# Kernel optimization log

Hardware: AMD Instinct MI355X
Metric: run time of the kernel (lower is better)

## Reference

```python
import jax, jax.numpy as jnp
import numpy as np

C = 256
C8 = C // 8
B, H, W = 8, 64, 64


def setup_inputs() -> dict:
    key = jax.random.key(0)
    ks = jax.random.split(key, 8)
    scale = 1.0 / np.sqrt(C)
    return {
        "x": jax.random.normal(ks[0], (B, C, H, W), dtype=jnp.float32),
        "wq": jax.random.normal(ks[1], (C8, C), dtype=jnp.float32) * scale,
        "bq": jax.random.normal(ks[2], (C8,), dtype=jnp.float32) * 0.01,
        "wk": jax.random.normal(ks[3], (C8, C), dtype=jnp.float32) * scale,
        "bk": jax.random.normal(ks[4], (C8,), dtype=jnp.float32) * 0.01,
        "wv": jax.random.normal(ks[5], (C, C), dtype=jnp.float32) * scale,
        "bv": jax.random.normal(ks[6], (C,), dtype=jnp.float32) * 0.01,
        "gamma": jax.random.normal(ks[7], (1,), dtype=jnp.float32) * 0.1,
    }


def reference(x, wq, bq, wk, bk, wv, bv, gamma):
    b, c, h, w = x.shape
    n = h * w
    xf = x.reshape(b, c, n)  # flatten spatial; 1x1 conv == channel matmul
    q = jnp.einsum('oc,bcn->bno', wq, xf) + bq            # [b, n, c/8]
    k = jnp.einsum('oc,bcn->bon', wk, xf) + bk[:, None]   # [b, c/8, n]
    v = jnp.einsum('oc,bcn->bon', wv, xf) + bv[:, None]   # [b, c, n]
    attn = jax.nn.softmax(jnp.einsum('bno,bom->bnm', q, k), axis=2)  # [b,n,n]
    out = jnp.einsum('bcm,bnm->bcn', v, attn).reshape(b, c, h, w)
    return x + gamma[0] * out
```

## Files before the change

### kernel.cpp

```cpp
#include <hip/hip_runtime.h>

typedef unsigned short ushort_t;
typedef __bf16 bf16x8 __attribute__((ext_vector_type(8)));
typedef float f32x16 __attribute__((ext_vector_type(16)));
typedef float f32x4 __attribute__((ext_vector_type(4)));
typedef unsigned int u32x4 __attribute__((ext_vector_type(4)));
typedef unsigned int u32x2 __attribute__((ext_vector_type(2)));

#define L2E 1.44269504088896340736f

__device__ __forceinline__ unsigned cvt_pk_bf16(float a, float b) {
  unsigned r;
  asm("v_cvt_pk_bf16_f32 %0, %1, %2" : "=v"(r) : "v"(a), "v"(b));
  return r;
}

__device__ __forceinline__ float fast_exp2(float v) {
#if __has_builtin(__builtin_amdgcn_exp2f)
  return __builtin_amdgcn_exp2f(v);
#else
  return exp2f(v);
#endif
}

__device__ __forceinline__ f32x16 mfma32(u32x4 a, u32x4 b, f32x16 c) {
  return __builtin_amdgcn_mfma_f32_32x32x16_bf16(
      __builtin_bit_cast(bf16x8, a), __builtin_bit_cast(bf16x8, b), c, 0, 0, 0);
}

__global__ __launch_bounds__(256, 1) void proj_kernel(
    const float* __restrict__ x,
    const float* __restrict__ wq, const float* __restrict__ bq,
    const float* __restrict__ wk, const float* __restrict__ bk,
    const float* __restrict__ wv, const float* __restrict__ bv,
    ushort_t* __restrict__ qtg, ushort_t* __restrict__ ktg,
    ushort_t* __restrict__ vtg)
{
  __shared__ ushort_t xT[128 * 256];
  __shared__ ushort_t wl[64 * 256];

  const int tid  = threadIdx.x;
  const int b    = blockIdx.x & 7;
  const int nt   = blockIdx.x >> 3;
  const int n0   = nt * 128;
  const int lane = tid & 63;
  const int wid  = tid >> 6;
  const int l31  = lane & 31;
  const int half = lane >> 5;

  {
    const int xn = tid & 127;
    const int ch = (tid >> 7) * 8;
    const float* xb = x + (size_t)b * 256 * 4096 + (n0 + xn);
    #pragma unroll
    for (int rep = 0; rep < 16; ++rep) {
      const int c0 = rep * 16 + ch;
      float f0 = xb[(size_t)(c0+0)*4096], f1 = xb[(size_t)(c0+1)*4096];
      float f2 = xb[(size_t)(c0+2)*4096], f3 = xb[(size_t)(c0+3)*4096];
      float f4 = xb[(size_t)(c0+4)*4096], f5 = xb[(size_t)(c0+5)*4096];
      float f6 = xb[(size_t)(c0+6)*4096], f7 = xb[(size_t)(c0+7)*4096];
      u32x4 pk;
      pk.x = cvt_pk_bf16(f0, f1); pk.y = cvt_pk_bf16(f2, f3);
      pk.z = cvt_pk_bf16(f4, f5); pk.w = cvt_pk_bf16(f6, f7);
      *(u32x4*)((char*)xT + xn*512 + ((c0*2) ^ ((xn & 7) << 4))) = pk;
    }
  }

  for (int oc = 0; oc < 5; ++oc) {
    __syncthreads();
    {
      const int r   = tid >> 2;
      const int row = oc*64 + r;
      const float* wrow = (row < 32) ? (wq + row*256)
                        : (row < 64) ? (wk + (row-32)*256)
                                     : (wv + (row-64)*256);
      #pragma unroll
      for (int rep = 0; rep < 4; ++rep) {
        const int c0 = ((tid & 3)*4 + rep) * 16;
        f32x4 g0 = *(const f32x4*)(wrow + c0);
        f32x4 g1 = *(const f32x4*)(wrow + c0 + 4);
        f32x4 g2 = *(const f32x4*)(wrow + c0 + 8);
        f32x4 g3 = *(const f32x4*)(wrow + c0 + 12);
        u32x4 pa, pb;
        pa.x = cvt_pk_bf16(g0.x, g0.y); pa.y = cvt_pk_bf16(g0.z, g0.w);
        pa.z = cvt_pk_bf16(g1.x, g1.y); pa.w = cvt_pk_bf16(g1.z, g1.w);
        pb.x = cvt_pk_bf16(g2.x, g2.y); pb.y = cvt_pk_bf16(g2.z, g2.w);
        pb.z = cvt_pk_bf16(g3.x, g3.y); pb.w = cvt_pk_bf16(g3.z, g3.w);
        *(u32x4*)((char*)wl + r*512 + ((c0*2)     ^ ((r & 7) << 4))) = pa;
        *(u32x4*)((char*)wl + r*512 + (((c0+8)*2) ^ ((r & 7) << 4))) = pb;
      }
    }
    __syncthreads();

    f32x16 acc0 = {}, acc1 = {};
    const int nloc = wid*32 + l31;
    #pragma unroll
    for (int kc = 0; kc < 16; ++kc) {
      const int cb = kc*16 + half*8;
      u32x4 bf = *(const u32x4*)((const char*)xT + nloc*512      + ((cb*2) ^ ((nloc & 7) << 4)));
      u32x4 a0 = *(const u32x4*)((const char*)wl + l31*512       + ((cb*2) ^ ((l31  & 7) << 4)));
      u32x4 a1 = *(const u32x4*)((const char*)wl + (32+l31)*512  + ((cb*2) ^ ((l31  & 7) << 4)));
      acc0 = mfma32(a0, bf, acc0);
      acc1 = mfma32(a1, bf, acc1);
    }

    const int nglob = n0 + wid*32 + l31;
    #pragma unroll
    for (int ot = 0; ot < 2; ++ot) {
      f32x16 acc = ot ? acc1 : acc0;
      if (oc == 0) {
        ushort_t* dst = ot ? ktg : qtg;
        const float* bias = ot ? bk : bq;
        const size_t rowbase = ((size_t)b*4096 + nglob) * 32;
        #pragma unroll
        for (int g = 0; g < 4; ++g) {
          const int ob = 8*g + 4*half;
          float v0 = acc[4*g+0] + bias[ob+0];
          float v1 = acc[4*g+1] + bias[ob+1];
          float v2 = acc[4*g+2] + bias[ob+2];
          float v3 = acc[4*g+3] + bias[ob+3];
          u32x2 pk2; pk2.x = cvt_pk_bf16(v0, v1); pk2.y = cvt_pk_bf16(v2, v3);
          *(u32x2*)(dst + rowbase + ob) = pk2;
        }
      } else {
        const int cbase = oc*64 - 64 + ot*32;
        #pragma unroll
        for (int r = 0; r < 16; ++r) {
          const int c = cbase + (r & 3) + 8*(r >> 2) + 4*half;
          float v = acc[r] + bv[c];
          vtg[((size_t)b*256 + c)*4096 + nglob] = (ushort_t)cvt_pk_bf16(v, v);
        }
      }
    }
  }
}

__global__ __launch_bounds__(256, 1) void attn_kernel(
    const ushort_t* __restrict__ qtg, const ushort_t* __restrict__ ktg,
    const ushort_t* __restrict__ vtg, const float* __restrict__ x,
    const float* __restrict__ gamma, float* __restrict__ out)
{
  __shared__ ushort_t vtile[2][8192];

  const int tid  = threadIdx.x;
  const int lane = tid & 63;
  const int wid  = tid >> 6;
  const int l31  = lane & 31;
  const int half = lane >> 5;
  const int b    = blockIdx.x & 7;
  const int qt   = blockIdx.x >> 3;
  const int n0   = qt*128 + wid*32;
  const int nq   = n0 + l31;

  const ushort_t* qrow = qtg + ((size_t)b*4096 + nq)*32;
  const u32x4 q0 = *(const u32x4*)(qrow + half*8);
  const u32x4 q1 = *(const u32x4*)(qrow + 16 + half*8);

  const ushort_t* ktb = ktg + (size_t)b*4096*32;
  const ushort_t* vgb = vtg + (size_t)b*256*4096;

  const int srow = lane >> 2;
  const int scol = lane & 3;

  #pragma unroll
  for (int j = 0; j < 4; ++j) {
    const int cr = wid*64 + j*16 + srow;
    const int gs = scol ^ ((cr >> 1) & 3);
    const ushort_t* gp = vgb + (size_t)cr*4096 + gs*8;
    const ushort_t* lp = &vtile[0][0] + (wid*4 + j)*512;
    __builtin_amdgcn_global_load_lds((const __attribute__((address_space(1))) void*)gp,
                                     (__attribute__((address_space(3))) void*)lp, 16, 0, 0);
  }
  u32x4 kf0 = *(const u32x4*)(ktb + (size_t)l31*32 + half*8);
  u32x4 kf1 = *(const u32x4*)(ktb + (size_t)l31*32 + 16 + half*8);
  asm volatile("s_waitcnt vmcnt(0)" ::: "memory");
  __syncthreads();

  float mrun = -3.0e38f, lrun = 0.0f;
  f32x16 oacc[8] = {};
  u32x4 kn0 = q0, kn1 = q1;

  #pragma unroll 2
  for (int t = 0; t < 128; ++t) {
    const int cur = t & 1;
    const char* vb = (const char*)&vtile[0][0] + cur*16384;

    u32x4 vf0[8], vf1[8];
    #pragma unroll
    for (int ct = 0; ct < 8; ++ct) {
      const int cr = ct*32 + l31;
      const int sw = (cr >> 1) & 3;
      vf0[ct] = *(const u32x4*)(vb + cr*64 + ((half ^ sw) << 4));
      vf1[ct] = *(const u32x4*)(vb + cr*64 + (((2 + half) ^ sw) << 4));
    }

    if (t < 127) {
      const int m1 = (t + 1) * 32;
      #pragma unroll
      for (int j = 0; j < 4; ++j) {
        const int cr = wid*64 + j*16 + srow;
        const int gs = scol ^ ((cr >> 1) & 3);
        const ushort_t* gp = vgb + (size_t)cr*4096 + m1 + gs*8;
        const ushort_t* lp = &vtile[0][0] + (cur ^ 1)*8192 + (wid*4 + j)*512;
        __builtin_amdgcn_global_load_lds((const __attribute__((address_space(1))) void*)gp,
                                         (__attribute__((address_space(3))) void*)lp, 16, 0, 0);
      }
      const ushort_t* kr = ktb + (size_t)(m1 + l31)*32;
      kn0 = *(const u32x4*)(kr + half*8);
      kn1 = *(const u32x4*)(kr + 16 + half*8);
    }

    f32x16 s = {};
    s = mfma32(kf0, q0, s);
    s = mfma32(kf1, q1, s);

    float x0 = fmaxf(s[0],  s[1]),  x1 = fmaxf(s[2],  s[3]);
    float x2 = fmaxf(s[4],  s[5]),  x3 = fmaxf(s[6],  s[7]);
    float x4 = fmaxf(s[8],  s[9]),  x5 = fmaxf(s[10], s[11]);
    float x6 = fmaxf(s[12], s[13]), x7 = fmaxf(s[14], s[15]);
    x0 = fmaxf(x0, x1); x2 = fmaxf(x2, x3);
    x4 = fmaxf(x4, x5); x6 = fmaxf(x6, x7);
    x0 = fmaxf(x0, x2); x4 = fmaxf(x4, x6);
    const float vmx  = fmaxf(x0, x4);
    const float pmax = fmaxf(vmx, __shfl_xor(vmx, 32, 64));

    if (__any(pmax > mrun + 8.0f)) {
      const float mnew = fmaxf(mrun, pmax);
      const float sc   = fast_exp2((mrun - mnew) * L2E);
      lrun *= sc;
      #pragma unroll
      for (int ct = 0; ct < 8; ++ct)
        #pragma unroll
        for (int r = 0; r < 16; ++r) oacc[ct][r] *= sc;
      mrun = mnew;
    }

    const float ml2 = mrun * L2E;
    float p[16];
    #pragma unroll
    for (int r = 0; r < 16; ++r) p[r] = fast_exp2(fmaf(s[r], L2E, -ml2));
    const float ps = (((p[0]+p[1])+(p[2]+p[3])) + ((p[4]+p[5])+(p[6]+p[7])))
                   + (((p[8]+p[9])+(p[10]+p[11])) + ((p[12]+p[13])+(p[14]+p[15])));
    lrun += ps + __shfl_xor(ps, 32, 64);

    const unsigned wd0 = cvt_pk_bf16(p[0],  p[1]),  wd1 = cvt_pk_bf16(p[2],  p[3]);
    const unsigned wd2 = cvt_pk_bf16(p[4],  p[5]),  wd3 = cvt_pk_bf16(p[6],  p[7]);
    const unsigned wd4 = cvt_pk_bf16(p[8],  p[9]),  wd5 = cvt_pk_bf16(p[10], p[11]);
    const unsigned wd6 = cvt_pk_bf16(p[12], p[13]), wd7 = cvt_pk_bf16(p[14], p[15]);
    const unsigned pw0 = __shfl_xor((int)wd0, 32, 64), pw1 = __shfl_xor((int)wd1, 32, 64);
    const unsigned pw2 = __shfl_xor((int)wd2, 32, 64), pw3 = __shfl_xor((int)wd3, 32, 64);
    const unsigned pw4 = __shfl_xor((int)wd4, 32, 64), pw5 = __shfl_xor((int)wd5, 32, 64);
    const unsigned pw6 = __shfl_xor((int)wd6, 32, 64), pw7 = __shfl_xor((int)wd7, 32, 64);
    u32x4 pb0, pb1;
    pb0.x = half ? pw2 : wd0;  pb0.y = half ? pw3 : wd1;
    pb0.z = half ? wd2 : pw0;  pb0.w = half ? wd3 : pw1;
    pb1.x = half ? pw6 : wd4;  pb1.y = half ? pw7 : wd5;
    pb1.z = half ? wd6 : pw4;  pb1.w = half ? wd7 : pw5;

    #pragma unroll
    for (int ct = 0; ct < 8; ++ct) {
      oacc[ct] = mfma32(vf0[ct], pb0, oacc[ct]);
      oacc[ct] = mfma32(vf1[ct], pb1, oacc[ct]);
    }

    asm volatile("s_waitcnt vmcnt(0)" ::: "memory");
    __syncthreads();
    kf0 = kn0; kf1 = kn1;
  }

  const float inv_l = 1.0f / lrun;
  const float g = gamma[0];
  const size_t xoff = (size_t)b*256*4096 + (size_t)(qt*128 + wid*32 + l31);
  const float* xb = x + xoff;
  float* ob = out + xoff;
  #pragma unroll
  for (int ct = 0; ct < 8; ++ct) {
    #pragma unroll
    for (int r = 0; r < 16; ++r) {
      const int c = ct*32 + (r & 3) + 8*(r >> 2) + 4*half;
      const size_t off = (size_t)c * 4096;
      ob[off] = xb[off] + g * (oacc[ct][r] * inv_l);
    }
  }
}

extern "C" void kernel_launch(void* const* d_in, const int* in_sizes, int n_in,
                              void* d_out, int out_size, void* d_ws, size_t ws_size,
                              hipStream_t stream) {
  (void)in_sizes; (void)n_in; (void)out_size; (void)ws_size;
  const float* x     = (const float*)d_in[0];
  const float* wq    = (const float*)d_in[1];
  const float* bq    = (const float*)d_in[2];
  const float* wk    = (const float*)d_in[3];
  const float* bk    = (const float*)d_in[4];
  const float* wv    = (const float*)d_in[5];
  const float* bv    = (const float*)d_in[6];
  const float* gamma = (const float*)d_in[7];
  float* out = (float*)d_out;

  ushort_t* ws  = (ushort_t*)d_ws;
  ushort_t* qtw = ws;
  ushort_t* ktw = ws + (size_t)8*4096*32;
  ushort_t* vww = ws + (size_t)2*8*4096*32;

  proj_kernel<<<256, 256, 0, stream>>>(x, wq, bq, wk, bk, wv, bv, qtw, ktw, vww);
  attn_kernel<<<256, 256, 0, stream>>>(qtw, ktw, vww, x, gamma, out);
}
```

Before: 255.4 us.

## Repartition attention across 8 waves by query pairs and channel quarters, stage K in LDS

The attention kernel now runs 512 threads per block. Each wave handles two 32-query tiles and a 64-channel slice of the output, instead of one query tile across all 256 channels. K tiles are staged into LDS with global_load_lds alongside V, and the MFMA sections are wrapped in s_setprio. The projection kernel uses 64-column tiles, giving 512 blocks and a 2-blocks-per-CU launch bound, and loads weights with narrower vectors. The aim is more waves in flight and less register pressure per wave, at the cost of recomputing the QK scores and softmax in each of the four channel-slice waves.

Result: slower. 333.8 us (+30.7%).

```diff
diff --git a/kernel.cpp b/kernel.cpp
--- a/kernel.cpp
+++ b/kernel.cpp
@@ -3,7 +3,7 @@
 typedef unsigned short ushort_t;
 typedef __bf16 bf16x8 __attribute__((ext_vector_type(8)));
 typedef float f32x16 __attribute__((ext_vector_type(16)));
-typedef float f32x4 __attribute__((ext_vector_type(4)));
+typedef float f32x4v __attribute__((ext_vector_type(4)));
 typedef unsigned int u32x4 __attribute__((ext_vector_type(4)));
 typedef unsigned int u32x2 __attribute__((ext_vector_type(2)));
 
@@ -23,12 +23,20 @@
 #endif
 }
 
+__device__ __forceinline__ float cross_half_max(float v) {
+  return fmaxf(v, __shfl_xor(v, 32, 64));
+}
+
+__device__ __forceinline__ float cross_half_sum(float v) {
+  return v + __shfl_xor(v, 32, 64);
+}
+
 __device__ __forceinline__ f32x16 mfma32(u32x4 a, u32x4 b, f32x16 c) {
   return __builtin_amdgcn_mfma_f32_32x32x16_bf16(
       __builtin_bit_cast(bf16x8, a), __builtin_bit_cast(bf16x8, b), c, 0, 0, 0);
 }
 
-__global__ __launch_bounds__(256, 1) void proj_kernel(
+__global__ __launch_bounds__(256, 2) void proj_kernel(
     const float* __restrict__ x,
     const float* __restrict__ wq, const float* __restrict__ bq,
     const float* __restrict__ wk, const float* __restrict__ bk,
@@ -36,25 +44,27 @@
     ushort_t* __restrict__ qtg, ushort_t* __restrict__ ktg,
     ushort_t* __restrict__ vtg)
 {
-  __shared__ ushort_t xT[128 * 256];
+  __shared__ ushort_t xT[64 * 256];
   __shared__ ushort_t wl[64 * 256];
 
   const int tid  = threadIdx.x;
   const int b    = blockIdx.x & 7;
   const int nt   = blockIdx.x >> 3;
-  const int n0   = nt * 128;
+  const int n0   = nt * 64;
   const int lane = tid & 63;
   const int wid  = tid >> 6;
   const int l31  = lane & 31;
   const int half = lane >> 5;
+  const int nh   = wid & 1;
+  const int oh   = wid >> 1;
 
   {
-    const int xn = tid & 127;
-    const int ch = (tid >> 7) * 8;
+    const int xn   = tid & 63;
+    const int cgrp = tid >> 6;
     const float* xb = x + (size_t)b * 256 * 4096 + (n0 + xn);
     #pragma unroll
-    for (int rep = 0; rep < 16; ++rep) {
-      const int c0 = rep * 16 + ch;
+    for (int j = 0; j < 8; ++j) {
+      const int c0 = cgrp * 64 + j * 8;
       float f0 = xb[(size_t)(c0+0)*4096], f1 = xb[(size_t)(c0+1)*4096];
       float f2 = xb[(size_t)(c0+2)*4096], f3 = xb[(size_t)(c0+3)*4096];
       float f4 = xb[(size_t)(c0+4)*4096], f5 = xb[(size_t)(c0+5)*4096];
@@ -68,218 +78,212 @@
 
   for (int oc = 0; oc < 5; ++oc) {
     __syncthreads();
-    {
-      const int r   = tid >> 2;
-      const int row = oc*64 + r;
-      const float* wrow = (row < 32) ? (wq + row*256)
-                        : (row < 64) ? (wk + (row-32)*256)
-                                     : (wv + (row-64)*256);
-      #pragma unroll
-      for (int rep = 0; rep < 4; ++rep) {
-        const int c0 = ((tid & 3)*4 + rep) * 16;
-        f32x4 g0 = *(const f32x4*)(wrow + c0);
-        f32x4 g1 = *(const f32x4*)(wrow + c0 + 4);
-        f32x4 g2 = *(const f32x4*)(wrow + c0 + 8);
-        f32x4 g3 = *(const f32x4*)(wrow + c0 + 12);
-        u32x4 pa, pb;
-        pa.x = cvt_pk_bf16(g0.x, g0.y); pa.y = cvt_pk_bf16(g0.z, g0.w);
-        pa.z = cvt_pk_bf16(g1.x, g1.y); pa.w = cvt_pk_bf16(g1.z, g1.w);
-        pb.x = cvt_pk_bf16(g2.x, g2.y); pb.y = cvt_pk_bf16(g2.z, g2.w);
-        pb.z = cvt_pk_bf16(g3.x, g3.y); pb.w = cvt_pk_bf16(g3.z, g3.w);
-        *(u32x4*)((char*)wl + r*512 + ((c0*2)     ^ ((r & 7) << 4))) = pa;
-        *(u32x4*)((char*)wl + r*512 + (((c0+8)*2) ^ ((r & 7) << 4))) = pb;
-      }
+    #pragma unroll
+    for (int i = 0; i < 16; ++i) {
+      const int lin4 = i * 256 + tid;
+      const int row  = lin4 >> 6;
+      const int c4   = (lin4 & 63) * 4;
+      const int grow = oc * 64 + row;
+      const float* wrow = (grow < 32) ? (wq + grow*256)
+                        : (grow < 64) ? (wk + (grow-32)*256)
+                                      : (wv + (grow-64)*256);
+      f32x4v g = *(const f32x4v*)(wrow + c4);
+      u32x2 pk2; pk2.x = cvt_pk_bf16(g.x, g.y); pk2.y = cvt_pk_bf16(g.z, g.w);
+      *(u32x2*)((char*)wl + row*512 + ((c4*2) ^ ((row & 7) << 4))) = pk2;
     }
     __syncthreads();
 
-    f32x16 acc0 = {}, acc1 = {};
-    const int nloc = wid*32 + l31;
+    f32x16 acc = {};
+    const int nloc = nh*32 + l31;
+    const int oloc = oh*32 + l31;
     #pragma unroll
     for (int kc = 0; kc < 16; ++kc) {
       const int cb = kc*16 + half*8;
-      u32x4 bf = *(const u32x4*)((const char*)xT + nloc*512      + ((cb*2) ^ ((nloc & 7) << 4)));
-      u32x4 a0 = *(const u32x4*)((const char*)wl + l31*512       + ((cb*2) ^ ((l31  & 7) << 4)));
-      u32x4 a1 = *(const u32x4*)((const char*)wl + (32+l31)*512  + ((cb*2) ^ ((l31  & 7) << 4)));
-      acc0 = mfma32(a0, bf, acc0);
-      acc1 = mfma32(a1, bf, acc1);
-    }
-
-    const int nglob = n0 + wid*32 + l31;
-    #pragma unroll
-    for (int ot = 0; ot < 2; ++ot) {
-      f32x16 acc = ot ? acc1 : acc0;
-      if (oc == 0) {
-        ushort_t* dst = ot ? ktg : qtg;
-        const float* bias = ot ? bk : bq;
-        const size_t rowbase = ((size_t)b*4096 + nglob) * 32;
-        #pragma unroll
-        for (int g = 0; g < 4; ++g) {
-          const int ob = 8*g + 4*half;
-          float v0 = acc[4*g+0] + bias[ob+0];
-          float v1 = acc[4*g+1] + bias[ob+1];
-          float v2 = acc[4*g+2] + bias[ob+2];
-          float v3 = acc[4*g+3] + bias[ob+3];
-          u32x2 pk2; pk2.x = cvt_pk_bf16(v0, v1); pk2.y = cvt_pk_bf16(v2, v3);
-          *(u32x2*)(dst + rowbase + ob) = pk2;
-        }
-      } else {
-        const int cbase = oc*64 - 64 + ot*32;
-        #pragma unroll
-        for (int r = 0; r < 16; ++r) {
-          const int c = cbase + (r & 3) + 8*(r >> 2) + 4*half;
-          float v = acc[r] + bv[c];
-          vtg[((size_t)b*256 + c)*4096 + nglob] = (ushort_t)cvt_pk_bf16(v, v);
-        }
-      }
-    }
-  }
-}
-
-__global__ __launch_bounds__(256, 1) void attn_kernel(
+      u32x4 bf = *(const u32x4*)((const char*)xT + nloc*512 + ((cb*2) ^ ((nloc & 7) << 4)));
+      u32x4 af = *(const u32x4*)((const char*)wl + oloc*512 + ((cb*2) ^ ((oloc & 7) << 4)));
+      acc = mfma32(af, bf, acc);
+    }
+
+    const int nglob = n0 + nh*32 + l31;
+    if (oc == 0) {
+      ushort_t* dst = oh ? ktg : qtg;
+      const float* bias = oh ? bk : bq;
+      const size_t rowbase = ((size_t)b*4096 + nglob) * 32;
+      #pragma unroll
+      for (int g = 0; g < 4; ++g) {
+        const int ob = 8*g + 4*half;
+        float v0 = acc[4*g+0] + bias[ob+0];
+        float v1 = acc[4*g+1] + bias[ob+1];
+        float v2 = acc[4*g+2] + bias[ob+2];
+        float v3 = acc[4*g+3] + bias[ob+3];
+        u32x2 pk2; pk2.x = cvt_pk_bf16(v0, v1); pk2.y = cvt_pk_bf16(v2, v3);
+        *(u32x2*)(dst + rowbase + ob) = pk2;
+      }
+    } else {
+      const int cbase = (oc-1)*64 + oh*32;
+      #pragma unroll
+      for (int r = 0; r < 16; ++r) {
+        const int c = cbase + (r & 3) + 8*(r >> 2) + 4*half;
+        float v = acc[r] + bv[c];
+        vtg[((size_t)b*256 + c)*4096 + nglob] = (ushort_t)cvt_pk_bf16(v, v);
+      }
+    }
+  }
+}
+
+__global__ __launch_bounds__(512, 2) void attn_kernel(
     const ushort_t* __restrict__ qtg, const ushort_t* __restrict__ ktg,
     const ushort_t* __restrict__ vtg, const float* __restrict__ x,
     const float* __restrict__ gamma, float* __restrict__ out)
 {
-  __shared__ ushort_t vtile[2][8192];
+  __shared__ ushort_t vls[2 * 8192];
+  __shared__ ushort_t kls[2 * 1024];
 
   const int tid  = threadIdx.x;
   const int lane = tid & 63;
   const int wid  = tid >> 6;
   const int l31  = lane & 31;
   const int half = lane >> 5;
+  const int qg   = wid & 1;
+  const int ch   = wid >> 1;
   const int b    = blockIdx.x & 7;
   const int qt   = blockIdx.x >> 3;
-  const int n0   = qt*128 + wid*32;
-  const int nq   = n0 + l31;
-
-  const ushort_t* qrow = qtg + ((size_t)b*4096 + nq)*32;
-  const u32x4 q0 = *(const u32x4*)(qrow + half*8);
-  const u32x4 q1 = *(const u32x4*)(qrow + 16 + half*8);
+  const int qbase = qt*128 + qg*64;
 
   const ushort_t* ktb = ktg + (size_t)b*4096*32;
   const ushort_t* vgb = vtg + (size_t)b*256*4096;
 
-  const int srow = lane >> 2;
-  const int scol = lane & 3;
-
+  u32x4 qf[2][2];
   #pragma unroll
-  for (int j = 0; j < 4; ++j) {
-    const int cr = wid*64 + j*16 + srow;
-    const int gs = scol ^ ((cr >> 1) & 3);
-    const ushort_t* gp = vgb + (size_t)cr*4096 + gs*8;
-    const ushort_t* lp = &vtile[0][0] + (wid*4 + j)*512;
-    __builtin_amdgcn_global_load_lds((const __attribute__((address_space(1))) void*)gp,
-                                     (__attribute__((address_space(3))) void*)lp, 16, 0, 0);
-  }
-  u32x4 kf0 = *(const u32x4*)(ktb + (size_t)l31*32 + half*8);
-  u32x4 kf1 = *(const u32x4*)(ktb + (size_t)l31*32 + 16 + half*8);
+  for (int qt2 = 0; qt2 < 2; ++qt2) {
+    const ushort_t* qrow = qtg + ((size_t)b*4096 + qbase + qt2*32 + l31)*32;
+    qf[qt2][0] = *(const u32x4*)(qrow + half*8);
+    qf[qt2][1] = *(const u32x4*)(qrow + 16 + half*8);
+  }
+
+  #define STAGE_TILE(nb, t) do {                                              \
+    _Pragma("unroll")                                                         \
+    for (int i = 0; i < 2; ++i) {                                             \
+      const ushort_t* gp = vgb + (size_t)(wid*32 + l31)*4096 + (t)*32 + (i*2+half)*8; \
+      const ushort_t* lp = vls + (nb)*8192 + wid*1024 + i*512;                \
+      __builtin_amdgcn_global_load_lds(                                       \
+          (const __attribute__((address_space(1))) void*)gp,                  \
+          (__attribute__((address_space(3))) void*)lp, 16, 0, 0);             \
+    }                                                                         \
+    if (wid < 2) {                                                            \
+      const ushort_t* gp = ktb + (size_t)((t)*32 + l31)*32 + wid*16 + half*8; \
+      const ushort_t* lp = kls + (nb)*1024 + wid*512;                         \
+      __builtin_amdgcn_global_load_lds(                                       \
+          (const __attribute__((address_space(1))) void*)gp,                  \
+          (__attribute__((address_space(3))) void*)lp, 16, 0, 0);             \
+    }                                                                         \
+  } while (0)
+
+  STAGE_TILE(0, 0);
   asm volatile("s_waitcnt vmcnt(0)" ::: "memory");
   __syncthreads();
 
-  float mrun = -3.0e38f, lrun = 0.0f;
-  f32x16 oacc[8] = {};
-  u32x4 kn0 = q0, kn1 = q1;
+  float mrun[2] = {-3.0e38f, -3.0e38f};
+  float lrun[2] = {0.0f, 0.0f};
+  f32x16 oacc[4] = {};
 
   #pragma unroll 2
   for (int t = 0; t < 128; ++t) {
     const int cur = t & 1;
-    const char* vb = (const char*)&vtile[0][0] + cur*16384;
-
-    u32x4 vf0[8], vf1[8];
-    #pragma unroll
-    for (int ct = 0; ct < 8; ++ct) {
-      const int cr = ct*32 + l31;
-      const int sw = (cr >> 1) & 3;
-      vf0[ct] = *(const u32x4*)(vb + cr*64 + ((half ^ sw) << 4));
-      vf1[ct] = *(const u32x4*)(vb + cr*64 + (((2 + half) ^ sw) << 4));
-    }
-
-    if (t < 127) {
-      const int m1 = (t + 1) * 32;
-      #pragma unroll
-      for (int j = 0; j < 4; ++j) {
-        const int cr = wid*64 + j*16 + srow;
-        const int gs = scol ^ ((cr >> 1) & 3);
-        const ushort_t* gp = vgb + (size_t)cr*4096 + m1 + gs*8;
-        const ushort_t* lp = &vtile[0][0] + (cur ^ 1)*8192 + (wid*4 + j)*512;
-        __builtin_amdgcn_global_load_lds((const __attribute__((address_space(1))) void*)gp,
-                                         (__attribute__((address_space(3))) void*)lp, 16, 0, 0);
-      }
-      const ushort_t* kr = ktb + (size_t)(m1 + l31)*32;
-      kn0 = *(const u32x4*)(kr + half*8);
-      kn1 = *(const u32x4*)(kr + 16 + half*8);
-    }
-
-    f32x16 s = {};
-    s = mfma32(kf0, q0, s);
-    s = mfma32(kf1, q1, s);
-
-    float x0 = fmaxf(s[0],  s[1]),  x1 = fmaxf(s[2],  s[3]);
-    float x2 = fmaxf(s[4],  s[5]),  x3 = fmaxf(s[6],  s[7]);
-    float x4 = fmaxf(s[8],  s[9]),  x5 = fmaxf(s[10], s[11]);
-    float x6 = fmaxf(s[12], s[13]), x7 = fmaxf(s[14], s[15]);
-    x0 = fmaxf(x0, x1); x2 = fmaxf(x2, x3);
-    x4 = fmaxf(x4, x5); x6 = fmaxf(x6, x7);
-    x0 = fmaxf(x0, x2); x4 = fmaxf(x4, x6);
-    const float vmx  = fmaxf(x0, x4);
-    const float pmax = fmaxf(vmx, __shfl_xor(vmx, 32, 64));
-
-    if (__any(pmax > mrun + 8.0f)) {
-      const float mnew = fmaxf(mrun, pmax);
-      const float sc   = fast_exp2((mrun - mnew) * L2E);
-      lrun *= sc;
-      #pragma unroll
-      for (int ct = 0; ct < 8; ++ct)
+
+    if (t < 127) STAGE_TILE(cur ^ 1, t + 1);
+
+    const char* kb = (const char*)kls + cur*2048;
+    const u32x4 kf0 = *(const u32x4*)(kb + half*512 + l31*16);
+    const u32x4 kf1 = *(const u32x4*)(kb + 1024 + half*512 + l31*16);
+
+    const char* vb = (const char*)vls + cur*16384;
+    u32x4 vf[2][2];
+    #pragma unroll
+    for (int ct = 0; ct < 2; ++ct)
+      #pragma unroll
+      for (int mh = 0; mh < 2; ++mh)
+        vf[ct][mh] = *(const u32x4*)(vb + (((ch*2+ct)*4 + mh*2 + half)*32 + l31)*16);
+
+    f32x16 s0 = {}, s1 = {};
+    __builtin_amdgcn_s_setprio(1);
+    s0 = mfma32(kf0, qf[0][0], s0);  s0 = mfma32(kf1, qf[0][1], s0);
+    s1 = mfma32(kf0, qf[1][0], s1);  s1 = mfma32(kf1, qf[1][1], s1);
+    __builtin_amdgcn_s_setprio(0);
+
+    u32x4 pb[2][2];
+    #pragma unroll
+    for (int qt2 = 0; qt2 < 2; ++qt2) {
+      const f32x16 s = qt2 ? s1 : s0;
+      float x0 = fmaxf(fmaxf(s[0],  s[1]),  fmaxf(s[2],  s[3]));
+      float x1 = fmaxf(fmaxf(s[4],  s[5]),  fmaxf(s[6],  s[7]));
+      float x2 = fmaxf(fmaxf(s[8],  s[9]),  fmaxf(s[10], s[11]));
+      float x3 = fmaxf(fmaxf(s[12], s[13]), fmaxf(s[14], s[15]));
+      const float vmx  = fmaxf(fmaxf(x0, x1), fmaxf(x2, x3));
+      const float pmax = cross_half_max(vmx);
+
+      if (__any(pmax > mrun[qt2] + 8.0f)) {
+        const float mnew = fmaxf(mrun[qt2], pmax);
+        const float sc   = fast_exp2((mrun[qt2] - mnew) * L2E);
+        lrun[qt2] *= sc;
         #pragma unroll
-        for (int r = 0; r < 16; ++r) oacc[ct][r] *= sc;
-      mrun = mnew;
-    }
-
-    const float ml2 = mrun * L2E;
-    float p[16];
-    #pragma unroll
-    for (int r = 0; r < 16; ++r) p[r] = fast_exp2(fmaf(s[r], L2E, -ml2));
-    const float ps = (((p[0]+p[1])+(p[2]+p[3])) + ((p[4]+p[5])+(p[6]+p[7])))
-                   + (((p[8]+p[9])+(p[10]+p[11])) + ((p[12]+p[13])+(p[14]+p[15])));
-    lrun += ps + __shfl_xor(ps, 32, 64);
-
-    const unsigned wd0 = cvt_pk_bf16(p[0],  p[1]),  wd1 = cvt_pk_bf16(p[2],  p[3]);
-    const unsigned wd2 = cvt_pk_bf16(p[4],  p[5]),  wd3 = cvt_pk_bf16(p[6],  p[7]);
-    const unsigned wd4 = cvt_pk_bf16(p[8],  p[9]),  wd5 = cvt_pk_bf16(p[10], p[11]);
-    const unsigned wd6 = cvt_pk_bf16(p[12], p[13]), wd7 = cvt_pk_bf16(p[14], p[15]);
-    const unsigned pw0 = __shfl_xor((int)wd0, 32, 64), pw1 = __shfl_xor((int)wd1, 32, 64);
-    const unsigned pw2 = __shfl_xor((int)wd2, 32, 64), pw3 = __shfl_xor((int)wd3, 32, 64);
-    const unsigned pw4 = __shfl_xor((int)wd4, 32, 64), pw5 = __shfl_xor((int)wd5, 32, 64);
-    const unsigned pw6 = __shfl_xor((int)wd6, 32, 64), pw7 = __shfl_xor((int)wd7, 32, 64);
-    u32x4 pb0, pb1;
-    pb0.x = half ? pw2 : wd0;  pb0.y = half ? pw3 : wd1;
-    pb0.z = half ? wd2 : pw0;  pb0.w = half ? wd3 : pw1;
-    pb1.x = half ? pw6 : wd4;  pb1.y = half ? pw7 : wd5;
-    pb1.z = half ? wd6 : pw4;  pb1.w = half ? wd7 : pw5;
-
-    #pragma unroll
-    for (int ct = 0; ct < 8; ++ct) {
-      oacc[ct] = mfma32(vf0[ct], pb0, oacc[ct]);
-      oacc[ct] = mfma32(vf1[ct], pb1, oacc[ct]);
-    }
+        for (int ct = 0; ct < 2; ++ct)
+          #pragma unroll
+          for (int r = 0; r < 16; ++r) oacc[qt2*2+ct][r] *= sc;
+        mrun[qt2] = mnew;
+      }
+
+      const float ml2 = mrun[qt2] * L2E;
+      float p[16];
+      #pragma unroll
+      for (int r = 0; r < 16; ++r) p[r] = fast_exp2(fmaf(s[r], L2E, -ml2));
+      const float ps = (((p[0]+p[1])+(p[2]+p[3])) + ((p[4]+p[5])+(p[6]+p[7])))
+                     + (((p[8]+p[9])+(p[10]+p[11])) + ((p[12]+p[13])+(p[14]+p[15])));
+      lrun[qt2] += cross_half_sum(ps);
+
+      const unsigned wd0 = cvt_pk_bf16(p[0],  p[1]),  wd1 = cvt_pk_bf16(p[2],  p[3]);
+      const unsigned wd2 = cvt_pk_bf16(p[4],  p[5]),  wd3 = cvt_pk_bf16(p[6],  p[7]);
+      const unsigned wd4 = cvt_pk_bf16(p[8],  p[9]),  wd5 = cvt_pk_bf16(p[10], p[11]);
+      const unsigned wd6 = cvt_pk_bf16(p[12], p[13]), wd7 = cvt_pk_bf16(p[14], p[15]);
+      const unsigned pw0 = __shfl_xor((int)wd0, 32, 64), pw1 = __shfl_xor((int)wd1, 32, 64);
+      const unsigned pw2 = __shfl_xor((int)wd2, 32, 64), pw3 = __shfl_xor((int)wd3, 32, 64);
+      const unsigned pw4 = __shfl_xor((int)wd4, 32, 64), pw5 = __shfl_xor((int)wd5, 32, 64);
+      const unsigned pw6 = __shfl_xor((int)wd6, 32, 64), pw7 = __shfl_xor((int)wd7, 32, 64);
+      pb[qt2][0].x = half ? pw2 : wd0;  pb[qt2][0].y = half ? pw3 : wd1;
+      pb[qt2][0].z = half ? wd2 : pw0;  pb[qt2][0].w = half ? wd3 : pw1;
+      pb[qt2][1].x = half ? pw6 : wd4;  pb[qt2][1].y = half ? pw7 : wd5;
+      pb[qt2][1].z = half ? wd6 : pw4;  pb[qt2][1].w = half ? wd7 : pw5;
+    }
+
+    __builtin_amdgcn_s_setprio(1);
+    #pragma unroll
+    for (int qt2 = 0; qt2 < 2; ++qt2)
+      #pragma unroll
+      for (int ct = 0; ct < 2; ++ct) {
+        oacc[qt2*2+ct] = mfma32(vf[ct][0], pb[qt2][0], oacc[qt2*2+ct]);
+        oacc[qt2*2+ct] = mfma32(vf[ct][1], pb[qt2][1], oacc[qt2*2+ct]);
+      }
+    __builtin_amdgcn_s_setprio(0);
 
     asm volatile("s_waitcnt vmcnt(0)" ::: "memory");
     __syncthreads();
-    kf0 = kn0; kf1 = kn1;
-  }
-
-  const float inv_l = 1.0f / lrun;
+  }
+
   const float g = gamma[0];
-  const size_t xoff = (size_t)b*256*4096 + (size_t)(qt*128 + wid*32 + l31);
-  const float* xb = x + xoff;
-  float* ob = out + xoff;
   #pragma unroll
-  for (int ct = 0; ct < 8; ++ct) {
-    #pragma unroll
-    for (int r = 0; r < 16; ++r) {
-      const int c = ct*32 + (r & 3) + 8*(r >> 2) + 4*half;
-      const size_t off = (size_t)c * 4096;
-      ob[off] = xb[off] + g * (oacc[ct][r] * inv_l);
+  for (int qt2 = 0; qt2 < 2; ++qt2) {
+    const float inv_l = 1.0f / lrun[qt2];
+    const size_t nglob = qbase + qt2*32 + l31;
+    const float* xb = x   + (size_t)b*256*4096 + nglob;
+    float*       ob = out + (size_t)b*256*4096 + nglob;
+    #pragma unroll
+    for (int ct = 0; ct < 2; ++ct) {
+      #pragma unroll
+      for (int r = 0; r < 16; ++r) {
+        const int c = ch*64 + ct*32 + (r & 3) + 8*(r >> 2) + 4*half;
+        const size_t off = (size_t)c * 4096;
+        ob[off] = xb[off] + g * (oacc[qt2*2+ct][r] * inv_l);
+      }
     }
   }
 }
@@ -303,6 +307,6 @@
   ushort_t* ktw = ws + (size_t)8*4096*32;
   ushort_t* vww = ws + (size_t)2*8*4096*32;
 
-  proj_kernel<<<256, 256, 0, stream>>>(x, wq, bq, wk, bk, wv, bv, qtw, ktw, vww);
-  attn_kernel<<<256, 256, 0, stream>>>(qtw, ktw, vww, x, gamma, out);
-}
+  proj_kernel<<<512, 256, 0, stream>>>(x, wq, bq, wk, bk, wv, bv, qtw, ktw, vww);
+  attn_kernel<<<256, 512, 0, stream>>>(qtw, ktw, vww, x, gamma, out);
+}
```
